# Optimization experiments

Hardware: AMD Instinct MI355X
Metric: run time of the kernel (lower is better)

## Reference

```python
import jax, jax.numpy as jnp
import numpy as np

N = 1024      # num nodes
IN = 128      # input_dim
H = 128       # hidden_dim
E = 32768     # num edges (avg degree 32)


def setup_inputs() -> dict:
    key = jax.random.key(0)
    ks = jax.random.split(key, 16)
    def w(k, shape, fan_in):
        return (jax.random.normal(k, shape, jnp.float32) / np.sqrt(fan_in)).astype(jnp.float32)
    return {
        "x": jax.random.normal(ks[0], (N, IN), jnp.float32),
        "edge_index": jax.random.randint(ks[1], (2, E), 0, N, dtype=jnp.int32),
        # GCNConv layers: weight [in, out] (applied as x @ W), bias [out]
        "conv0_w": w(ks[2], (IN, H), IN), "conv0_b": w(ks[3], (H,), IN),
        "conv1_w": w(ks[4], (H, H), H),   "conv1_b": w(ks[5], (H,), H),
        "conv2_w": w(ks[6], (H, H), H),   "conv2_b": w(ks[7], (H,), H),
        # output Linear
        "out_w": w(ks[8], (H, H), H), "out_b": w(ks[9], (H,), H),
        # distance predictor: Linear(2H->H), ReLU, Linear(H->1), Sigmoid
        "dp_w1": w(ks[10], (H, 2 * H), 2 * H), "dp_b1": w(ks[11], (H,), 2 * H),
        "dp_w2": w(ks[12], (1, H), H),         "dp_b2": w(ks[13], (1,), H),
    }


def gcn_conv(x, edge_index, W, b):
    """PyG GCNConv: add self-loops, symmetric normalization, sum-aggregate."""
    n = x.shape[0]
    loop = jnp.arange(n, dtype=edge_index.dtype)
    src = jnp.concatenate([edge_index[0], loop])
    dst = jnp.concatenate([edge_index[1], loop])
    xw = x @ W                                            # [N, out]
    deg = jax.ops.segment_sum(jnp.ones_like(dst, jnp.float32), dst, num_segments=n)
    dinv = jnp.where(deg > 0, jax.lax.rsqrt(jnp.maximum(deg, 1.0)), 0.0)
    norm = dinv[src] * dinv[dst]                          # [E+N]
    out = jax.ops.segment_sum(xw[src] * norm[:, None], dst, num_segments=n)
    return out + b


def pairwise_distances(emb, dp_w1, dp_b1, dp_w2, dp_b2):
    # Linear on concat([e_i, e_j]) decomposes: W1 @ [e_i; e_j] = e_i @ A^T + e_j @ B^T
    h = emb.shape[1]
    u = emb @ dp_w1[:, :h].T                              # [N, H] (contribution of e_i)
    v = emb @ dp_w1[:, h:].T                              # [N, H] (contribution of e_j)
    hid = jax.nn.relu(u[:, None, :] + v[None, :, :] + dp_b1)  # [N, N, H]
    p = jax.nn.sigmoid(jnp.einsum('ijh,h->ij', hid, dp_w2[0]) + dp_b2[0])  # [N, N]
    # loop fills only i<j then mirrors; diagonal stays 0
    upper = jnp.triu(p, k=1)
    return upper + upper.T


def reference(x, edge_index, conv0_w, conv0_b, conv1_w, conv1_b, conv2_w, conv2_b,
              out_w, out_b, dp_w1, dp_b1, dp_w2, dp_b2):
    h = gcn_conv(x, edge_index, conv0_w, conv0_b)
    h = jax.nn.relu(h)  # dropout is identity in eval mode
    h = gcn_conv(h, edge_index, conv1_w, conv1_b)
    h = jax.nn.relu(h)
    h = gcn_conv(h, edge_index, conv2_w, conv2_b)
    node_embeddings = h @ out_w + out_b
    distances = pairwise_distances(node_embeddings, dp_w1, dp_b1, dp_w2, dp_b2)
    return node_embeddings, distances
```

## Files before the change

### kernel.cpp

```cpp
#include <hip/hip_runtime.h>
#include <hip/hip_bf16.h>

#define NN 1024
#define HD 128
#define NE 32768
#define CAP 128


__global__ __launch_bounds__(256) void k_zero(int* __restrict__ deg,
                                              const float* __restrict__ dpw1,
                                              float* __restrict__ At,
                                              float* __restrict__ Bt) {
    int t = threadIdx.x;
    if (blockIdx.x == 0) {
#pragma unroll
        for (int i = t; i < NN; i += 256) deg[i] = 0;
    } else {
        int i = (blockIdx.x - 1) * 256 + t;
        for (; i < HD * 2 * HD; i += 64 * 256) {
            int h = i >> 8, k = i & 255;
            float v = dpw1[i];
            if (k < HD) At[k * HD + h] = v;
            else        Bt[(k - HD) * HD + h] = v;
        }
    }
}

__global__ __launch_bounds__(256) void k_mm0f(const float* __restrict__ x,
                                              const float* __restrict__ W0,
                                              const int* __restrict__ ei,
                                              int* __restrict__ deg,
                                              int* __restrict__ col,
                                              float* __restrict__ y) {
    int t = threadIdx.x;
    if (blockIdx.x < 512) {
        __shared__ float rows[2][HD];
        int half = t >> 7, h = t & 127;
        int n = blockIdx.x * 2 + half;
        rows[half][h] = x[n * HD + h];
        __syncthreads();
        float acc = 0.f;
#pragma unroll 8
        for (int k = 0; k < HD; k++) acc += rows[half][k] * W0[k * HD + h];
        y[n * HD + h] = acc;
    } else {
        int gid = (blockIdx.x - 512) * 256 + t;
        for (int e = gid; e < NE; e += 16 * 256) {
            int dst = ei[NE + e];
            int slot = atomicAdd(&deg[dst], 1);
            if (slot < CAP) col[dst * CAP + slot] = ei[e];
        }
    }
}

__global__ __launch_bounds__(256) void k_layer1(const float* __restrict__ yin,
                                                const int* __restrict__ deg,
                                                const int* __restrict__ col,
                                                const float* __restrict__ bias,
                                                const float* __restrict__ W,
                                                float* __restrict__ yout) {
    __shared__ float sdinv[NN];
    __shared__ float hrow[2][HD];
    __shared__ int   scol[2][CAP];
    int t = threadIdx.x;
    int half = t >> 7, h = t & 127;
    int n = blockIdx.x * 2 + half;
    for (int i = t; i < NN; i += 256) sdinv[i] = rsqrtf((float)deg[i] + 1.f);
    int cnt = deg[n];
    if (cnt > CAP) cnt = CAP;
    for (int i = h; i < cnt; i += 128) scol[half][i] = col[n * CAP + i];
    __syncthreads();
    float dvn = sdinv[n];
    float s0 = 0.f, s1 = 0.f, s2 = 0.f, s3 = 0.f;
    int i = 0;
    for (; i + 3 < cnt; i += 4) {
        int c0 = scol[half][i + 0], c1 = scol[half][i + 1];
        int c2 = scol[half][i + 2], c3 = scol[half][i + 3];
        s0 += sdinv[c0] * yin[c0 * HD + h];
        s1 += sdinv[c1] * yin[c1 * HD + h];
        s2 += sdinv[c2] * yin[c2 * HD + h];
        s3 += sdinv[c3] * yin[c3 * HD + h];
    }
    for (; i < cnt; i++) { int c = scol[half][i]; s0 += sdinv[c] * yin[c * HD + h]; }
    float s = dvn * yin[n * HD + h] + ((s0 + s1) + (s2 + s3));
    float hv = dvn * s + bias[h];
    hrow[half][h] = fmaxf(hv, 0.f);
    __syncthreads();
    float acc = 0.f;
#pragma unroll 8
    for (int k = 0; k < HD; k++) acc += hrow[half][k] * W[k * HD + h];
    yout[n * HD + h] = dvn * acc;
}

__global__ __launch_bounds__(256) void k_layer2(const float* __restrict__ yin,
                                                const int* __restrict__ deg,
                                                const int* __restrict__ col,
                                                const float* __restrict__ bias,
                                                const float* __restrict__ W,
                                                float* __restrict__ yout) {
    __shared__ float hrow[2][HD];
    __shared__ int   scol[2][CAP];
    int t = threadIdx.x;
    int half = t >> 7, h = t & 127;
    int n = blockIdx.x * 2 + half;
    int cnt = deg[n];
    if (cnt > CAP) cnt = CAP;
    float dvn = rsqrtf((float)cnt + 1.f);
    for (int i = h; i < cnt; i += 128) scol[half][i] = col[n * CAP + i];
    __syncthreads();
    float s0 = 0.f, s1 = 0.f, s2 = 0.f, s3 = 0.f;
    int i = 0;
    for (; i + 3 < cnt; i += 4) {
        int c0 = scol[half][i + 0], c1 = scol[half][i + 1];
        int c2 = scol[half][i + 2], c3 = scol[half][i + 3];
        s0 += yin[c0 * HD + h];
        s1 += yin[c1 * HD + h];
        s2 += yin[c2 * HD + h];
        s3 += yin[c3 * HD + h];
    }
    for (; i < cnt; i++) s0 += yin[scol[half][i] * HD + h];
    float s = yin[n * HD + h] + ((s0 + s1) + (s2 + s3));
    float hv = dvn * s + bias[h];
    hrow[half][h] = fmaxf(hv, 0.f);
    __syncthreads();
    float acc = 0.f;
#pragma unroll 8
    for (int k = 0; k < HD; k++) acc += hrow[half][k] * W[k * HD + h];
    yout[n * HD + h] = dvn * acc;
}

__global__ __launch_bounds__(256) void k_final(const float* __restrict__ yin,
                                               const int* __restrict__ deg,
                                               const int* __restrict__ col,
                                               const float* __restrict__ conv2_b,
                                               const float* __restrict__ out_w,
                                               const float* __restrict__ out_b,
                                               const float* __restrict__ At,
                                               const float* __restrict__ Bt,
                                               const float* __restrict__ dp_b1,
                                               float* __restrict__ emb_out,
                                               float* __restrict__ u,
                                               float* __restrict__ v) {
    __shared__ float h2row[2][HD];
    __shared__ float embrow[2][HD];
    __shared__ int   scol[2][CAP];
    int t = threadIdx.x;
    int half = t >> 7, h = t & 127;
    int n = blockIdx.x * 2 + half;
    int cnt = deg[n];
    if (cnt > CAP) cnt = CAP;
    float dvn = rsqrtf((float)cnt + 1.f);
    for (int i = h; i < cnt; i += 128) scol[half][i] = col[n * CAP + i];
    __syncthreads();
    float s0 = 0.f, s1 = 0.f, s2 = 0.f, s3 = 0.f;
    int i = 0;
    for (; i + 3 < cnt; i += 4) {
        int c0 = scol[half][i + 0], c1 = scol[half][i + 1];
        int c2 = scol[half][i + 2], c3 = scol[half][i + 3];
        s0 += yin[c0 * HD + h];
        s1 += yin[c1 * HD + h];
        s2 += yin[c2 * HD + h];
        s3 += yin[c3 * HD + h];
    }
    for (; i < cnt; i++) s0 += yin[scol[half][i] * HD + h];
    float s = yin[n * HD + h] + ((s0 + s1) + (s2 + s3));
    h2row[half][h] = dvn * s + conv2_b[h];
    __syncthreads();
    float acc = out_b[h];
#pragma unroll 8
    for (int k = 0; k < HD; k++) acc += h2row[half][k] * out_w[k * HD + h];
    embrow[half][h] = acc;
    emb_out[n * HD + h] = acc;
    __syncthreads();
    float uu = dp_b1[h], vv = 0.f;
#pragma unroll 8
    for (int k = 0; k < HD; k++) {
        float e = embrow[half][k];
        uu += e * At[k * HD + h];
        vv += e * Bt[k * HD + h];
    }
    u[n * HD + h] = uu;
    v[n * HD + h] = vv;
}

__global__ __launch_bounds__(256) void k_pair(const float* __restrict__ u,
                                              const float* __restrict__ v,
                                              const float* __restrict__ w2,
                                              const float* __restrict__ b2v,
                                              float* __restrict__ dist) {
    __shared__ float4 su4[32 * 32];
    __shared__ float4 sv4[32 * 32];
    __shared__ float4 sw24[32];
    __shared__ float sp[32][33];

    int t = threadIdx.x;
    int rem = blockIdx.x, bi = 0;
    while (rem >= 32 - bi) { rem -= 32 - bi; bi++; }
    int bj = bi + rem;
    int i0 = bi * 32, j0 = bj * 32;

#pragma unroll
    for (int r = 0; r < 4; r++) {
        int p = t + r * 256;
        int rowp = p >> 5, c = p & 31;
        su4[p] = *(const float4*)(u + (size_t)(i0 + rowp) * HD + (c << 2));
        sv4[c * 32 + rowp] = *(const float4*)(v + (size_t)(j0 + rowp) * HD + (c << 2));
    }
    if (t < 32) sw24[t] = *(const float4*)(w2 + 4 * t);
    __syncthreads();

    int jl = t & 31, ib = t >> 5;
    float acc0 = 0.f, acc1 = 0.f, acc2 = 0.f, acc3 = 0.f;
    for (int c = 0; c < 32; c++) {
        float4 vv = sv4[c * 32 + jl];
        float4 w4 = sw24[c];
        float4 a0 = su4[(ib * 4 + 0) * 32 + c];
        float4 a1 = su4[(ib * 4 + 1) * 32 + c];
        float4 a2 = su4[(ib * 4 + 2) * 32 + c];
        float4 a3 = su4[(ib * 4 + 3) * 32 + c];
        acc0 += fmaxf(a0.x + vv.x, 0.f) * w4.x + fmaxf(a0.y + vv.y, 0.f) * w4.y +
                fmaxf(a0.z + vv.z, 0.f) * w4.z + fmaxf(a0.w + vv.w, 0.f) * w4.w;
        acc1 += fmaxf(a1.x + vv.x, 0.f) * w4.x + fmaxf(a1.y + vv.y, 0.f) * w4.y +
                fmaxf(a1.z + vv.z, 0.f) * w4.z + fmaxf(a1.w + vv.w, 0.f) * w4.w;
        acc2 += fmaxf(a2.x + vv.x, 0.f) * w4.x + fmaxf(a2.y + vv.y, 0.f) * w4.y +
                fmaxf(a2.z + vv.z, 0.f) * w4.z + fmaxf(a2.w + vv.w, 0.f) * w4.w;
        acc3 += fmaxf(a3.x + vv.x, 0.f) * w4.x + fmaxf(a3.y + vv.y, 0.f) * w4.y +
                fmaxf(a3.z + vv.z, 0.f) * w4.z + fmaxf(a3.w + vv.w, 0.f) * w4.w;
    }
    float bb2 = b2v[0];
    float pr0 = 1.f / (1.f + __expf(-(acc0 + bb2)));
    float pr1 = 1.f / (1.f + __expf(-(acc1 + bb2)));
    float pr2 = 1.f / (1.f + __expf(-(acc2 + bb2)));
    float pr3 = 1.f / (1.f + __expf(-(acc3 + bb2)));
    sp[ib * 4 + 0][jl] = pr0;
    sp[ib * 4 + 1][jl] = pr1;
    sp[ib * 4 + 2][jl] = pr2;
    sp[ib * 4 + 3][jl] = pr3;
    __syncthreads();

    if (bi < bj) {
        dist[(size_t)(i0 + ib * 4 + 0) * NN + j0 + jl] = pr0;
        dist[(size_t)(i0 + ib * 4 + 1) * NN + j0 + jl] = pr1;
        dist[(size_t)(i0 + ib * 4 + 2) * NN + j0 + jl] = pr2;
        dist[(size_t)(i0 + ib * 4 + 3) * NN + j0 + jl] = pr3;
#pragma unroll
        for (int p = 0; p < 4; p++) {
            int jrow = ib * 4 + p;
            dist[(size_t)(j0 + jrow) * NN + i0 + jl] = sp[jl][jrow];
        }
    } else {
#pragma unroll
        for (int p = 0; p < 4; p++) {
            int il = ib * 4 + p;
            float val = (il < jl) ? sp[il][jl] : ((il > jl) ? sp[jl][il] : 0.f);
            dist[(size_t)(i0 + il) * NN + j0 + jl] = val;
        }
    }
}

extern "C" void kernel_launch(void* const* d_in, const int* in_sizes, int n_in,
                              void* d_out, int out_size, void* d_ws, size_t ws_size,
                              hipStream_t stream) {
    const float* x    = (const float*)d_in[0];
    const int*   ei   = (const int*)d_in[1];
    const float* w0   = (const float*)d_in[2];
    const float* b0   = (const float*)d_in[3];
    const float* w1   = (const float*)d_in[4];
    const float* b1c  = (const float*)d_in[5];
    const float* w2c  = (const float*)d_in[6];
    const float* b2c  = (const float*)d_in[7];
    const float* ow   = (const float*)d_in[8];
    const float* ob   = (const float*)d_in[9];
    const float* dpw1 = (const float*)d_in[10];
    const float* dpb1 = (const float*)d_in[11];
    const float* dpw2 = (const float*)d_in[12];
    const float* dpb2 = (const float*)d_in[13];

    float* out_emb  = (float*)d_out;
    float* out_dist = out_emb + (size_t)NN * HD;

    char* p = (char*)d_ws;
    auto take = [&](size_t bytes) { void* r = p; p += (bytes + 255) & ~(size_t)255; return r; };
    int*   deg = (int*)take(NN * 4);
    int*   col = (int*)take(NN * CAP * 4);
    float* yA  = (float*)take(NN * HD * 4);
    float* yB  = (float*)take(NN * HD * 4);
    float* u   = (float*)take(NN * HD * 4);
    float* v   = (float*)take(NN * HD * 4);
    float* At  = (float*)take(HD * HD * 4);
    float* Bt  = (float*)take(HD * HD * 4);

    k_zero<<<65, 256, 0, stream>>>(deg, dpw1, At, Bt);
    k_mm0f<<<528, 256, 0, stream>>>(x, w0, ei, deg, col, yA);
    k_layer1<<<512, 256, 0, stream>>>(yA, deg, col, b0, w1, yB);
    k_layer2<<<512, 256, 0, stream>>>(yB, deg, col, b1c, w2c, yA);
    k_final<<<512, 256, 0, stream>>>(yA, deg, col, b2c, ow, ob, At, Bt, dpb1,
                                     out_emb, u, v);
    k_pair<<<(32 * 33) / 2, 256, 0, stream>>>(u, v, dpw2, dpb2, out_dist);
}
```

Measured before the change: 62.25 us.

## Build CSR with block-local shared atomics and aggregate before transform to drop a kernel

Edge bucketing now runs in a prep kernel where each of 32 blocks scans all edges and uses shared-memory atomics for its own 32 destination nodes. This replaces the global atomics and removes the separate degree zeroing. The GCN layers are reordered to aggregate first and apply the weight matrix afterwards, so the standalone x@W0 kernel goes away and the launch count drops from six to five. In exchange, every prep block reads the whole edge list, and the final kernel carries an extra matmul stage.

```diff
diff --git a/kernel.cpp b/kernel.cpp
--- a/kernel.cpp
+++ b/kernel.cpp
@@ -7,16 +7,29 @@
 #define CAP 128
 
 
-__global__ __launch_bounds__(256) void k_zero(int* __restrict__ deg,
+__global__ __launch_bounds__(256) void k_prep(const int* __restrict__ ei,
                                               const float* __restrict__ dpw1,
+                                              int* __restrict__ deg,
+                                              int* __restrict__ col,
                                               float* __restrict__ At,
                                               float* __restrict__ Bt) {
     int t = threadIdx.x;
-    if (blockIdx.x == 0) {
-#pragma unroll
-        for (int i = t; i < NN; i += 256) deg[i] = 0;
+    if (blockIdx.x < 32) {
+        int ob = blockIdx.x;
+        __shared__ int lcnt[32];
+        if (t < 32) lcnt[t] = 0;
+        __syncthreads();
+        for (int e = t; e < NE; e += 256) {
+            int dst = ei[NE + e];
+            if ((dst >> 5) == ob) {
+                int slot = atomicAdd(&lcnt[dst & 31], 1);
+                if (slot < CAP) col[dst * CAP + slot] = ei[e];
+            }
+        }
+        __syncthreads();
+        if (t < 32) deg[ob * 32 + t] = lcnt[t] < CAP ? lcnt[t] : CAP;
     } else {
-        int i = (blockIdx.x - 1) * 256 + t;
+        int i = (blockIdx.x - 32) * 256 + t;
         for (; i < HD * 2 * HD; i += 64 * 256) {
             int h = i >> 8, k = i & 255;
             float v = dpw1[i];
@@ -26,48 +39,20 @@
     }
 }
 
-__global__ __launch_bounds__(256) void k_mm0f(const float* __restrict__ x,
-                                              const float* __restrict__ W0,
-                                              const int* __restrict__ ei,
-                                              int* __restrict__ deg,
-                                              int* __restrict__ col,
-                                              float* __restrict__ y) {
-    int t = threadIdx.x;
-    if (blockIdx.x < 512) {
-        __shared__ float rows[2][HD];
-        int half = t >> 7, h = t & 127;
-        int n = blockIdx.x * 2 + half;
-        rows[half][h] = x[n * HD + h];
-        __syncthreads();
-        float acc = 0.f;
-#pragma unroll 8
-        for (int k = 0; k < HD; k++) acc += rows[half][k] * W0[k * HD + h];
-        y[n * HD + h] = acc;
-    } else {
-        int gid = (blockIdx.x - 512) * 256 + t;
-        for (int e = gid; e < NE; e += 16 * 256) {
-            int dst = ei[NE + e];
-            int slot = atomicAdd(&deg[dst], 1);
-            if (slot < CAP) col[dst * CAP + slot] = ei[e];
-        }
-    }
-}
-
-__global__ __launch_bounds__(256) void k_layer1(const float* __restrict__ yin,
-                                                const int* __restrict__ deg,
-                                                const int* __restrict__ col,
-                                                const float* __restrict__ bias,
-                                                const float* __restrict__ W,
-                                                float* __restrict__ yout) {
+__global__ __launch_bounds__(256) void k_l1(const float* __restrict__ x,
+                                            const int* __restrict__ deg,
+                                            const int* __restrict__ col,
+                                            const float* __restrict__ W0,
+                                            const float* __restrict__ b0,
+                                            float* __restrict__ s1out) {
     __shared__ float sdinv[NN];
-    __shared__ float hrow[2][HD];
+    __shared__ float aggrow[2][HD];
     __shared__ int   scol[2][CAP];
     int t = threadIdx.x;
     int half = t >> 7, h = t & 127;
     int n = blockIdx.x * 2 + half;
     for (int i = t; i < NN; i += 256) sdinv[i] = rsqrtf((float)deg[i] + 1.f);
     int cnt = deg[n];
-    if (cnt > CAP) cnt = CAP;
     for (int i = h; i < cnt; i += 128) scol[half][i] = col[n * CAP + i];
     __syncthreads();
     float dvn = sdinv[n];
@@ -76,35 +61,33 @@
     for (; i + 3 < cnt; i += 4) {
         int c0 = scol[half][i + 0], c1 = scol[half][i + 1];
         int c2 = scol[half][i + 2], c3 = scol[half][i + 3];
-        s0 += sdinv[c0] * yin[c0 * HD + h];
-        s1 += sdinv[c1] * yin[c1 * HD + h];
-        s2 += sdinv[c2] * yin[c2 * HD + h];
-        s3 += sdinv[c3] * yin[c3 * HD + h];
-    }
-    for (; i < cnt; i++) { int c = scol[half][i]; s0 += sdinv[c] * yin[c * HD + h]; }
-    float s = dvn * yin[n * HD + h] + ((s0 + s1) + (s2 + s3));
-    float hv = dvn * s + bias[h];
-    hrow[half][h] = fmaxf(hv, 0.f);
-    __syncthreads();
-    float acc = 0.f;
-#pragma unroll 8
-    for (int k = 0; k < HD; k++) acc += hrow[half][k] * W[k * HD + h];
-    yout[n * HD + h] = dvn * acc;
-}
-
-__global__ __launch_bounds__(256) void k_layer2(const float* __restrict__ yin,
-                                                const int* __restrict__ deg,
-                                                const int* __restrict__ col,
-                                                const float* __restrict__ bias,
-                                                const float* __restrict__ W,
-                                                float* __restrict__ yout) {
-    __shared__ float hrow[2][HD];
+        s0 += sdinv[c0] * x[c0 * HD + h];
+        s1 += sdinv[c1] * x[c1 * HD + h];
+        s2 += sdinv[c2] * x[c2 * HD + h];
+        s3 += sdinv[c3] * x[c3 * HD + h];
+    }
+    for (; i < cnt; i++) { int c = scol[half][i]; s0 += sdinv[c] * x[c * HD + h]; }
+    float s = dvn * x[n * HD + h] + ((s0 + s1) + (s2 + s3));
+    aggrow[half][h] = dvn * s;
+    __syncthreads();
+    float acc = b0[h];
+#pragma unroll 8
+    for (int k = 0; k < HD; k++) acc += aggrow[half][k] * W0[k * HD + h];
+    s1out[n * HD + h] = dvn * fmaxf(acc, 0.f);
+}
+
+__global__ __launch_bounds__(256) void k_l2(const float* __restrict__ s1in,
+                                            const int* __restrict__ deg,
+                                            const int* __restrict__ col,
+                                            const float* __restrict__ W1,
+                                            const float* __restrict__ b1,
+                                            float* __restrict__ s2out) {
+    __shared__ float aggrow[2][HD];
     __shared__ int   scol[2][CAP];
     int t = threadIdx.x;
     int half = t >> 7, h = t & 127;
     int n = blockIdx.x * 2 + half;
     int cnt = deg[n];
-    if (cnt > CAP) cnt = CAP;
     float dvn = rsqrtf((float)cnt + 1.f);
     for (int i = h; i < cnt; i += 128) scol[half][i] = col[n * CAP + i];
     __syncthreads();
@@ -113,42 +96,41 @@
     for (; i + 3 < cnt; i += 4) {
         int c0 = scol[half][i + 0], c1 = scol[half][i + 1];
         int c2 = scol[half][i + 2], c3 = scol[half][i + 3];
-        s0 += yin[c0 * HD + h];
-        s1 += yin[c1 * HD + h];
-        s2 += yin[c2 * HD + h];
-        s3 += yin[c3 * HD + h];
-    }
-    for (; i < cnt; i++) s0 += yin[scol[half][i] * HD + h];
-    float s = yin[n * HD + h] + ((s0 + s1) + (s2 + s3));
-    float hv = dvn * s + bias[h];
-    hrow[half][h] = fmaxf(hv, 0.f);
-    __syncthreads();
-    float acc = 0.f;
-#pragma unroll 8
-    for (int k = 0; k < HD; k++) acc += hrow[half][k] * W[k * HD + h];
-    yout[n * HD + h] = dvn * acc;
-}
-
-__global__ __launch_bounds__(256) void k_final(const float* __restrict__ yin,
-                                               const int* __restrict__ deg,
-                                               const int* __restrict__ col,
-                                               const float* __restrict__ conv2_b,
-                                               const float* __restrict__ out_w,
-                                               const float* __restrict__ out_b,
-                                               const float* __restrict__ At,
-                                               const float* __restrict__ Bt,
-                                               const float* __restrict__ dp_b1,
-                                               float* __restrict__ emb_out,
-                                               float* __restrict__ u,
-                                               float* __restrict__ v) {
-    __shared__ float h2row[2][HD];
-    __shared__ float embrow[2][HD];
+        s0 += s1in[c0 * HD + h];
+        s1 += s1in[c1 * HD + h];
+        s2 += s1in[c2 * HD + h];
+        s3 += s1in[c3 * HD + h];
+    }
+    for (; i < cnt; i++) s0 += s1in[scol[half][i] * HD + h];
+    float s = s1in[n * HD + h] + ((s0 + s1) + (s2 + s3));
+    aggrow[half][h] = dvn * s;
+    __syncthreads();
+    float acc = b1[h];
+#pragma unroll 8
+    for (int k = 0; k < HD; k++) acc += aggrow[half][k] * W1[k * HD + h];
+    s2out[n * HD + h] = dvn * fmaxf(acc, 0.f);
+}
+
+__global__ __launch_bounds__(256) void k_fin(const float* __restrict__ s2in,
+                                             const int* __restrict__ deg,
+                                             const int* __restrict__ col,
+                                             const float* __restrict__ W2,
+                                             const float* __restrict__ b2,
+                                             const float* __restrict__ out_w,
+                                             const float* __restrict__ out_b,
+                                             const float* __restrict__ At,
+                                             const float* __restrict__ Bt,
+                                             const float* __restrict__ dp_b1,
+                                             float* __restrict__ emb_out,
+                                             float* __restrict__ u,
+                                             float* __restrict__ v) {
+    __shared__ float bufA[2][HD];
+    __shared__ float bufB[2][HD];
     __shared__ int   scol[2][CAP];
     int t = threadIdx.x;
     int half = t >> 7, h = t & 127;
     int n = blockIdx.x * 2 + half;
     int cnt = deg[n];
-    if (cnt > CAP) cnt = CAP;
     float dvn = rsqrtf((float)cnt + 1.f);
     for (int i = h; i < cnt; i += 128) scol[half][i] = col[n * CAP + i];
     __syncthreads();
@@ -157,27 +139,32 @@
     for (; i + 3 < cnt; i += 4) {
         int c0 = scol[half][i + 0], c1 = scol[half][i + 1];
         int c2 = scol[half][i + 2], c3 = scol[half][i + 3];
-        s0 += yin[c0 * HD + h];
-        s1 += yin[c1 * HD + h];
-        s2 += yin[c2 * HD + h];
-        s3 += yin[c3 * HD + h];
-    }
-    for (; i < cnt; i++) s0 += yin[scol[half][i] * HD + h];
-    float s = yin[n * HD + h] + ((s0 + s1) + (s2 + s3));
-    h2row[half][h] = dvn * s + conv2_b[h];
-    __syncthreads();
-    float acc = out_b[h];
-#pragma unroll 8
-    for (int k = 0; k < HD; k++) acc += h2row[half][k] * out_w[k * HD + h];
-    embrow[half][h] = acc;
-    emb_out[n * HD + h] = acc;
+        s0 += s2in[c0 * HD + h];
+        s1 += s2in[c1 * HD + h];
+        s2 += s2in[c2 * HD + h];
+        s3 += s2in[c3 * HD + h];
+    }
+    for (; i < cnt; i++) s0 += s2in[scol[half][i] * HD + h];
+    float s = s2in[n * HD + h] + ((s0 + s1) + (s2 + s3));
+    bufA[half][h] = dvn * s;
+    __syncthreads();
+    float acc = b2[h];
+#pragma unroll 8
+    for (int k = 0; k < HD; k++) acc += bufA[half][k] * W2[k * HD + h];
+    bufB[half][h] = acc;
+    __syncthreads();
+    float e = out_b[h];
+#pragma unroll 8
+    for (int k = 0; k < HD; k++) e += bufB[half][k] * out_w[k * HD + h];
+    bufA[half][h] = e;
+    emb_out[n * HD + h] = e;
     __syncthreads();
     float uu = dp_b1[h], vv = 0.f;
 #pragma unroll 8
     for (int k = 0; k < HD; k++) {
-        float e = embrow[half][k];
-        uu += e * At[k * HD + h];
-        vv += e * Bt[k * HD + h];
+        float em = bufA[half][k];
+        uu += em * At[k * HD + h];
+        vv += em * Bt[k * HD + h];
     }
     u[n * HD + h] = uu;
     v[n * HD + h] = vv;
@@ -290,11 +277,10 @@
     float* At  = (float*)take(HD * HD * 4);
     float* Bt  = (float*)take(HD * HD * 4);
 
-    k_zero<<<65, 256, 0, stream>>>(deg, dpw1, At, Bt);
-    k_mm0f<<<528, 256, 0, stream>>>(x, w0, ei, deg, col, yA);
-    k_layer1<<<512, 256, 0, stream>>>(yA, deg, col, b0, w1, yB);
-    k_layer2<<<512, 256, 0, stream>>>(yB, deg, col, b1c, w2c, yA);
-    k_final<<<512, 256, 0, stream>>>(yA, deg, col, b2c, ow, ob, At, Bt, dpb1,
-                                     out_emb, u, v);
+    k_prep<<<96, 256, 0, stream>>>(ei, dpw1, deg, col, At, Bt);
+    k_l1<<<512, 256, 0, stream>>>(x, deg, col, w0, b0, yA);
+    k_l2<<<512, 256, 0, stream>>>(yA, deg, col, w1, b1c, yB);
+    k_fin<<<512, 256, 0, stream>>>(yB, deg, col, w2c, b2c, ow, ob, At, Bt, dpb1,
+                                   out_emb, u, v);
     k_pair<<<(32 * 33) / 2, 256, 0, stream>>>(u, v, dpw2, dpb2, out_dist);
 }
```

After: 88.57 us. +42.3%, slower.
